# Kernel optimization log

Hardware: AMD Instinct MI355X
Metric: run time of the kernel (lower is better)

Reference implementation:

```python
import jax, jax.numpy as jnp
import numpy as np

# tcnn Hash-grid config from TropicalHashGrid.__init__ defaults
L = 16          # n_levels
F = 2           # n_features_per_level
T = 19          # log2_hashmap_size
N_MIN = 16      # base_resolution
N_MAX = 2048
SCALE = 1.0
HASHMAP = 1 << T
B = 2.0 ** (np.log2(N_MAX * SCALE / N_MIN) / (L - 1))  # per-level scale
PRIMES = np.array([1, 2654435761, 805459861], dtype=np.uint32)
# 8 trilinear corner offsets in {0,1}^3
CORNERS = np.stack(np.meshgrid(*([np.arange(2)] * 3), indexing='ij'), axis=-1).reshape(8, 3)
N_POINTS = 2 ** 21


def _level_encode(x, tbl, scale, res, dense):
    """One hash-grid level: x [N,3], tbl [HASHMAP,F] -> [N,F]."""
    pos = x * scale + 0.5                      # tcnn convention
    pf = jnp.floor(pos)
    frac = pos - pf                            # [N,3]
    grid = pf.astype(jnp.int32)                # [N,3]
    idx = grid[:, None, :] + jnp.asarray(CORNERS, jnp.int32)[None]  # [N,8,3]
    if dense:
        # coarse level fits densely: stride indexing x + y*res + z*res^2
        idx = jnp.minimum(idx, res - 1)
        flat = idx[..., 0] + idx[..., 1] * res + idx[..., 2] * (res * res)
    else:
        # spatial hash: xor of coordinate * prime, masked to table size
        u = idx.astype(jnp.uint32)
        flat = ((u[..., 0] * PRIMES[0]) ^ (u[..., 1] * PRIMES[1]) ^ (u[..., 2] * PRIMES[2]))
        flat = (flat & jnp.uint32(HASHMAP - 1)).astype(jnp.int32)
    feats = tbl[flat]                          # [N,8,F] gather
    c = jnp.asarray(CORNERS, jnp.float32)
    w = jnp.prod(jnp.where(c[None] > 0, frac[:, None, :], 1.0 - frac[:, None, :]), axis=-1)  # [N,8]
    return jnp.einsum('nc,ncf->nf', w, feats)  # trilinear blend


def setup_inputs() -> dict:
    key = jax.random.key(0)
    k1, k2 = jax.random.split(key)
    x = jax.random.uniform(k1, (N_POINTS, 3), dtype=jnp.float32)  # coords in [0,1)^3
    # hash table params (tcnn inits ~U(-1e-4,1e-4); scaled randn equivalent scale)
    table = jax.random.normal(k2, (L, HASHMAP, F), dtype=jnp.float32) * 1e-4
    return {"x": x, "table": table}


def reference(x, table):
    outs = []
    for l in range(L):
        scale = float(N_MIN * (B ** l) - 1.0)   # grid_scale per tcnn/_marks
        res = int(np.ceil(scale)) + 1
        dense = (res ** 3) <= HASHMAP
        outs.append(_level_encode(x, table[l], scale, res, dense))
    return jnp.concatenate(outs, axis=-1)        # [N, L*F]
```

## Files before the change

kernel.cpp:

```cpp
#include <hip/hip_runtime.h>
#include <cstdint>
#include <cmath>


typedef float    f32x2 __attribute__((ext_vector_type(2)));
typedef float    f32x4 __attribute__((ext_vector_type(4)));
typedef uint32_t u32x2 __attribute__((ext_vector_type(2)));
typedef uint32_t u32x4 __attribute__((ext_vector_type(4)));
typedef _Float16 h16x2 __attribute__((ext_vector_type(2)));

#define NLEVELS 16
#define HASHMAP (1 << 19)
#define HMASK ((uint32_t)(HASHMAP - 1))
#define PRIME_Y 2654435761u
#define PRIME_Z 805459861u
#define F16SCALE 1024.0f
#define F16UNSCALE (1.0f / 1024.0f)

struct HGParams {
    float scale[NLEVELS];
    int   res[NLEVELS];
    int   dense[NLEVELS];
    int   dpk_off[NLEVELS];
    int   hq_off[NLEVELS];
    int   dq_off[NLEVELS];
};

__device__ __forceinline__ uint32_t sel4(u32x4 q, uint32_t k) {
    const uint32_t a = (k & 1u) ? q.y : q.x;
    const uint32_t b = (k & 1u) ? q.w : q.z;
    return (k & 2u) ? b : a;
}
__device__ __forceinline__ void unpack_h2(uint32_t w, float& lo, float& hi) {
    const h16x2 h = __builtin_bit_cast(h16x2, w);
    lo = (float)h.x; hi = (float)h.y;
}
__device__ __forceinline__ uint32_t pack_h2(float a, float b) {
    h16x2 h; h.x = (_Float16)a; h.y = (_Float16)b;
    return __builtin_bit_cast(uint32_t, h);
}

__global__ __launch_bounds__(256) void repack_hashed_f16(
    const f32x4* __restrict__ table2, uint32_t* __restrict__ hqw, HGParams p)
{
    const int l = blockIdx.y;
    if (p.hq_off[l] < 0) return;
    const f32x4* __restrict__ src = table2 + (size_t)l * (HASHMAP / 2);
    u32x2* __restrict__ dst = (u32x2*)(hqw + (size_t)p.hq_off[l] * 4);
    for (int k = blockIdx.x * 256 + threadIdx.x; k < HASHMAP / 2;
         k += gridDim.x * 256) {
        const f32x4 v = src[k];
        u32x2 w;
        w.x = pack_h2(v.x * F16SCALE, v.y * F16SCALE);
        w.y = pack_h2(v.z * F16SCALE, v.w * F16SCALE);
        dst[k] = w;
    }
}

__global__ __launch_bounds__(256) void repack_dense_f16(
    const f32x2* __restrict__ table, u32x4* __restrict__ dqt, HGParams p)
{
    const int l = blockIdx.y;
    if (p.dq_off[l] < 0) return;
    const int res = p.res[l];
    const int rm = res - 1;
    const int r2 = res * res;
    const int res3 = r2 * res;
    const f32x2* __restrict__ src = table + (size_t)l * HASHMAP;
    u32x4* __restrict__ dst = dqt + p.dq_off[l];
    for (int k = blockIdx.x * 256 + threadIdx.x; k < res3;
         k += gridDim.x * 256) {
        const int x = k % res;
        const int t = k / res;
        const int y = t % res;
        const int dx = (x < rm) ? 1 : 0;
        const int dy = (y < rm) ? res : 0;
        const f32x2 e00 = src[k];
        const f32x2 e10 = src[k + dx];
        const f32x2 e01 = src[k + dy];
        const f32x2 e11 = src[k + dx + dy];
        u32x4 w;
        w.x = pack_h2(e00.x * F16SCALE, e00.y * F16SCALE);
        w.y = pack_h2(e10.x * F16SCALE, e10.y * F16SCALE);
        w.z = pack_h2(e01.x * F16SCALE, e01.y * F16SCALE);
        w.w = pack_h2(e11.x * F16SCALE, e11.y * F16SCALE);
        dst[k] = w;
    }
}

__global__ __launch_bounds__(256) void repack_dense_k(
    const f32x2* __restrict__ table, f32x4* __restrict__ dpk, HGParams p)
{
    const int l = blockIdx.y;
    if (!p.dense[l] || p.dpk_off[l] < 0) return;
    const int res = p.res[l];
    const int res3 = res * res * res;
    const f32x2* __restrict__ src = table + (size_t)l * HASHMAP;
    f32x4* __restrict__ dst = dpk + p.dpk_off[l];
    for (int k = blockIdx.x * 256 + threadIdx.x; k < res3; k += gridDim.x * 256) {
        const f32x2 a = src[k];
        const f32x2 b = src[k + 1];
        f32x4 v; v.x = a.x; v.y = a.y; v.z = b.x; v.w = b.y;
        dst[k] = v;
    }
}

__global__ __launch_bounds__(256) void hashgrid_level(
    const float* __restrict__ x,
    const float* __restrict__ table,
    const f32x4* __restrict__ dpk,
    const u32x4* __restrict__ hq,
    const u32x4* __restrict__ dq,
    f32x2* __restrict__ dst,
    HGParams p,
    int npoints,
    size_t stride_l,
    size_t stride_n)
{
    __shared__ float sx[768];
    const int tid = threadIdx.x;
    const int base = blockIdx.x << 8;
    const int l = blockIdx.y;

    const int total = npoints * 3;
#pragma unroll
    for (int k = 0; k < 3; ++k) {
        const int li = tid + (k << 8);
        const int gi = base * 3 + li;
        sx[li] = (gi < total) ? x[gi] : 0.0f;
    }
    __syncthreads();

    const int n = base + tid;
    if (n >= npoints) return;

    const float scale = p.scale[l];
    const int   res   = p.res[l];
    const bool  dense = (p.dense[l] != 0);

    const float px = sx[tid * 3 + 0] * scale + 0.5f;
    const float py = sx[tid * 3 + 1] * scale + 0.5f;
    const float pz = sx[tid * 3 + 2] * scale + 0.5f;
    const float fx = floorf(px), fy = floorf(py), fz = floorf(pz);
    const float rx = px - fx,  ry = py - fy,  rz = pz - fz;
    const int ix = (int)fx, iy = (int)fy, iz = (int)fz;

    const f32x2* __restrict__ tbl =
        (const f32x2*)table + (size_t)l * (size_t)HASHMAP;

    const float wx0 = 1.0f - rx, wx1 = rx;
    const float wy_[2] = {1.0f - ry, ry};
    const float wz_[2] = {1.0f - rz, rz};

    float ax = 0.0f, ay = 0.0f;
    float osc = 1.0f;

    if (dense) {
        const int rm = res - 1;
        const int x0 = min(ix, rm);
        const int y0 = min(iy, rm);
        const int z0 = min(iz, rm), z1 = min(iz + 1, rm);
        const int r2 = res * res;
        if (dq && p.dq_off[l] >= 0) {
            osc = F16UNSCALE;
            const u32x4* __restrict__ dt = dq + p.dq_off[l];
            const int b = x0 + y0 * res;
            const u32x4 qa = dt[b + z0 * r2];
            const u32x4 qb = dt[b + z1 * r2];
            const float wy0 = wy_[0], wy1 = wy_[1];
            float a00x, a00y, a10x, a10y, a01x, a01y, a11x, a11y;
            unpack_h2(qa.x, a00x, a00y);
            unpack_h2(qa.y, a10x, a10y);
            unpack_h2(qa.z, a01x, a01y);
            unpack_h2(qa.w, a11x, a11y);
            const float bax = wy0 * (wx0 * a00x + wx1 * a10x)
                            + wy1 * (wx0 * a01x + wx1 * a11x);
            const float bay = wy0 * (wx0 * a00y + wx1 * a10y)
                            + wy1 * (wx0 * a01y + wx1 * a11y);
            float b00x, b00y, b10x, b10y, b01x, b01y, b11x, b11y;
            unpack_h2(qb.x, b00x, b00y);
            unpack_h2(qb.y, b10x, b10y);
            unpack_h2(qb.z, b01x, b01y);
            unpack_h2(qb.w, b11x, b11y);
            const float bbx = wy0 * (wx0 * b00x + wx1 * b10x)
                            + wy1 * (wx0 * b01x + wx1 * b11x);
            const float bby = wy0 * (wx0 * b00y + wx1 * b10y)
                            + wy1 * (wx0 * b01y + wx1 * b11y);
            ax = wz_[0] * bax + wz_[1] * bbx;
            ay = wz_[0] * bay + wz_[1] * bby;
        } else {
            const int x1 = min(ix + 1, rm);
            const int yy1 = min(iy + 1, rm);
            const int ys[2] = {y0 * res, yy1 * res};
            const int zs[2] = {z0 * r2,  z1 * r2};
            const int d = x1 - x0;
            if (dpk && p.dpk_off[l] >= 0) {
                const f32x4* __restrict__ dt = dpk + p.dpk_off[l];
                f32x4 f4[4];
#pragma unroll
                for (int c = 0; c < 4; ++c)
                    f4[c] = dt[x0 + ys[(c >> 1) & 1] + zs[c & 1]];
#pragma unroll
                for (int c = 0; c < 4; ++c) {
                    const f32x2 c0 = f4[c].xy;
                    const f32x2 c1 = d ? f4[c].zw : f4[c].xy;
                    const float wyz = wy_[(c >> 1) & 1] * wz_[c & 1];
                    ax += wyz * (wx0 * c0.x + wx1 * c1.x);
                    ay += wyz * (wx0 * c0.y + wx1 * c1.y);
                }
            } else {
                f32x2 f0[4], f1[4];
#pragma unroll
                for (int c = 0; c < 4; ++c) {
                    const int b = ys[(c >> 1) & 1] + zs[c & 1];
                    f0[c] = tbl[x0 + b];
                    f1[c] = tbl[x1 + b];
                }
#pragma unroll
                for (int c = 0; c < 4; ++c) {
                    const float wyz = wy_[(c >> 1) & 1] * wz_[c & 1];
                    ax += wyz * (wx0 * f0[c].x + wx1 * f1[c].x);
                    ay += wyz * (wx0 * f0[c].y + wx1 * f1[c].y);
                }
            }
        }
    } else {
        const uint32_t ux = (uint32_t)ix;
        const uint32_t hy[2] = {(uint32_t)iy * PRIME_Y, (uint32_t)(iy + 1) * PRIME_Y};
        const uint32_t hz[2] = {(uint32_t)iz * PRIME_Z, (uint32_t)(iz + 1) * PRIME_Z};

        uint32_t H0[4], H1[4];
#pragma unroll
        for (int c = 0; c < 4; ++c) {
            const uint32_t hyz = hy[(c >> 1) & 1] ^ hz[c & 1];
            H0[c] = (ux ^ hyz) & HMASK;
            H1[c] = ((ux + 1u) ^ hyz) & HMASK;
        }

        if (hq && p.hq_off[l] >= 0) {
            osc = F16UNSCALE;
            const u32x4* __restrict__ ht = hq + p.hq_off[l];
            u32x4 q0[4];
#pragma unroll
            for (int c = 0; c < 4; ++c) q0[c] = ht[H0[c] >> 2];
            const bool straddle = ((ux & 3u) == 3u);
            u32x4 q1[4];
            if (straddle) {
#pragma unroll
                for (int c = 0; c < 4; ++c) q1[c] = ht[H1[c] >> 2];
            }
#pragma unroll
            for (int c = 0; c < 4; ++c) {
                const uint32_t e0 = sel4(q0[c], H0[c] & 3u);
                uint32_t e1;
                if (straddle) e1 = sel4(q1[c], H1[c] & 3u);
                else          e1 = sel4(q0[c], H1[c] & 3u);
                float c0x, c0y, c1x, c1y;
                unpack_h2(e0, c0x, c0y);
                unpack_h2(e1, c1x, c1y);
                const float wyz = wy_[(c >> 1) & 1] * wz_[c & 1];
                ax += wyz * (wx0 * c0x + wx1 * c1x);
                ay += wyz * (wx0 * c0y + wx1 * c1y);
            }
        } else {
            const f32x4* __restrict__ t4 = (const f32x4*)tbl;
            f32x4 f4[4];
#pragma unroll
            for (int c = 0; c < 4; ++c) f4[c] = t4[H0[c] >> 1];
            f32x2 c1v[4];
            if (ux & 1u) {
#pragma unroll
                for (int c = 0; c < 4; ++c) c1v[c] = tbl[H1[c]];
            } else {
#pragma unroll
                for (int c = 0; c < 4; ++c)
                    c1v[c] = (H0[c] & 1u) ? f4[c].xy : f4[c].zw;
            }
#pragma unroll
            for (int c = 0; c < 4; ++c) {
                const f32x2 c0 = (H0[c] & 1u) ? f4[c].zw : f4[c].xy;
                const float wyz = wy_[(c >> 1) & 1] * wz_[c & 1];
                ax += wyz * (wx0 * c0.x + wx1 * c1v[c].x);
                ay += wyz * (wx0 * c0.y + wx1 * c1v[c].y);
            }
        }
    }

    f32x2 acc; acc.x = ax * osc; acc.y = ay * osc;
    __builtin_nontemporal_store(acc, dst + (size_t)l * stride_l + (size_t)n * stride_n);
}

__global__ __launch_bounds__(256) void transpose_out(
    const f32x4* __restrict__ ws4,
    f32x4* __restrict__ out4,
    int npoints)
{
    __shared__ f32x2 tile[NLEVELS][130];
    const int tid = threadIdx.x;
    const int base = blockIdx.x << 7;
    const int np2 = npoints >> 1;

#pragma unroll
    for (int k = 0; k < 4; ++k) {
        const int flat = tid + (k << 8);
        const int l  = flat >> 6;
        const int pr = flat & 63;
        const int gp = (base >> 1) + pr;
        if (gp < np2) {
            const f32x4 v = __builtin_nontemporal_load(ws4 + (size_t)l * np2 + gp);
            tile[l][2 * pr]     = v.xy;
            tile[l][2 * pr + 1] = v.zw;
        }
    }
    __syncthreads();

#pragma unroll
    for (int k = 0; k < 4; ++k) {
        const int flat = tid + (k << 8);
        const int nl = flat >> 3;
        const int c  = flat & 7;
        const int nn = base + nl;
        if (nn < npoints) {
            const f32x2 a = tile[2 * c][nl];
            const f32x2 b = tile[2 * c + 1][nl];
            f32x4 v; v.x = a.x; v.y = a.y; v.z = b.x; v.w = b.y;
            __builtin_nontemporal_store(v, out4 + (size_t)nn * 8 + c);
        }
    }
}

extern "C" void kernel_launch(void* const* d_in, const int* in_sizes, int n_in,
                              void* d_out, int out_size, void* d_ws, size_t ws_size,
                              hipStream_t stream) {
    const float* x     = (const float*)d_in[0];
    const float* table = (const float*)d_in[1];
    float* out         = (float*)d_out;
    const int npoints  = in_sizes[0] / 3;

    HGParams p;
    const double B = pow(2.0, 7.0 / 15.0);
    int dpk_total = 0;
    int dq_total = 0;
    int hq_total = 0;
    int max_res3 = 0;
    for (int l = 0; l < NLEVELS; ++l) {
        const double s = 16.0 * pow(B, (double)l) - 1.0;
        p.scale[l] = (float)s;
        const int res = (int)ceil(s) + 1;
        p.res[l] = res;
        const long long r3 = (long long)res * res * res;
        p.dense[l] = (r3 <= (long long)HASHMAP) ? 1 : 0;
        if (p.dense[l]) {
            p.dpk_off[l] = dpk_total;  dpk_total += (int)r3;
            p.dq_off[l]  = dq_total;   dq_total  += (int)r3;
            p.hq_off[l]  = -1;
            if ((int)r3 > max_res3) max_res3 = (int)r3;
        } else {
            p.dpk_off[l] = -1;
            p.dq_off[l]  = -1;
            p.hq_off[l]  = hq_total;   hq_total  += HASHMAP / 4;
        }
    }

    const size_t need_main = (size_t)npoints * NLEVELS * sizeof(f32x2);
    const bool ws_main = (ws_size >= need_main) && ((npoints & 1) == 0);
    const size_t off0 = ws_main ? need_main : 0;

    const size_t hq_bytes = (size_t)hq_total * 16;
    const size_t dq_bytes = (size_t)dq_total * 16;
    const bool tierA = (ws_size >= off0 + hq_bytes + dq_bytes);

    const u32x4* hq = nullptr;
    const u32x4* dq = nullptr;
    const f32x4* dpk = nullptr;

    if (tierA) {
        uint32_t* hqw = (uint32_t*)((char*)d_ws + off0);
        u32x4*    dqt = (u32x4*)((char*)d_ws + off0 + hq_bytes);
        hq = (const u32x4*)hqw;
        dq = dqt;
        {
            const dim3 gr(1024, NLEVELS);
            repack_hashed_f16<<<gr, 256, 0, stream>>>(
                (const f32x4*)table, hqw, p);
        }
        {
            const dim3 gr((max_res3 + 255) / 256, NLEVELS);
            repack_dense_f16<<<gr, 256, 0, stream>>>(
                (const f32x2*)table, dqt, p);
        }
    } else {
        for (int l = 0; l < NLEVELS; ++l) { p.hq_off[l] = -1; p.dq_off[l] = -1; }
        const size_t need_dpk = (size_t)dpk_total * sizeof(f32x4);
        const bool use_dpk = (ws_size >= off0 + need_dpk) && dpk_total > 0;
        if (use_dpk) {
            f32x4* dpkw = (f32x4*)((char*)d_ws + off0);
            dpk = dpkw;
            const dim3 gr((max_res3 + 255) / 256, NLEVELS);
            repack_dense_k<<<gr, 256, 0, stream>>>((const f32x2*)table, dpkw, p);
        } else {
            for (int l = 0; l < NLEVELS; ++l) p.dpk_off[l] = -1;
        }
    }

    const dim3 g1((npoints + 255) / 256, NLEVELS);
    if (ws_main) {
        hashgrid_level<<<g1, 256, 0, stream>>>(
            x, table, dpk, hq, dq, (f32x2*)d_ws, p, npoints,
            (size_t)npoints, (size_t)1);
        const int nb2 = (npoints + 127) / 128;
        transpose_out<<<nb2, 256, 0, stream>>>(
            (const f32x4*)d_ws, (f32x4*)out, npoints);
    } else {
        hashgrid_level<<<g1, 256, 0, stream>>>(
            x, table, dpk, hq, dq, (f32x2*)out, p, npoints,
            (size_t)1, (size_t)NLEVELS);
    }
}
```

Measured before the change: 929.3 us.

## Process two points per thread to raise memory-level parallelism in hash gathers

Each thread now handles two consecutive points, issuing all gathers for both before blending so more loads are in flight per thread. The fp16 hashed path fetches only the single extra word on a straddle (via XOR of the x-delta) instead of a second full 16-byte row. Output is written as one 16-byte store when contiguous, and launch bounds request 8 waves per EU. This raises register pressure and halves the thread count, which may reduce latency hiding.

Result: slower. 1.020 ms (+9.7%).

```diff
diff --git a/kernel.cpp b/kernel.cpp
--- a/kernel.cpp
+++ b/kernel.cpp
@@ -105,7 +105,89 @@
     }
 }
 
-__global__ __launch_bounds__(256) void hashgrid_level(
+__device__ __forceinline__ void point_fp32(
+    const f32x2* __restrict__ tbl, const f32x4* __restrict__ dpkt,
+    bool dense, int res,
+    float rx, float ry, float rz, int ix, int iy, int iz,
+    float& ox, float& oy)
+{
+    const float wx0 = 1.0f - rx, wx1 = rx;
+    const float wy_[2] = {1.0f - ry, ry};
+    const float wz_[2] = {1.0f - rz, rz};
+    float ax = 0.0f, ay = 0.0f;
+    if (dense) {
+        const int rm = res - 1;
+        const int x0 = min(ix, rm), x1 = min(ix + 1, rm);
+        const int y0 = min(iy, rm), y1 = min(iy + 1, rm);
+        const int z0 = min(iz, rm), z1 = min(iz + 1, rm);
+        const int r2 = res * res;
+        const int ys[2] = {y0 * res, y1 * res};
+        const int zs[2] = {z0 * r2,  z1 * r2};
+        const int d = x1 - x0;
+        if (dpkt) {
+            f32x4 f4[4];
+#pragma unroll
+            for (int c = 0; c < 4; ++c)
+                f4[c] = dpkt[x0 + ys[(c >> 1) & 1] + zs[c & 1]];
+#pragma unroll
+            for (int c = 0; c < 4; ++c) {
+                const f32x2 c0 = f4[c].xy;
+                const f32x2 c1 = d ? f4[c].zw : f4[c].xy;
+                const float wyz = wy_[(c >> 1) & 1] * wz_[c & 1];
+                ax += wyz * (wx0 * c0.x + wx1 * c1.x);
+                ay += wyz * (wx0 * c0.y + wx1 * c1.y);
+            }
+        } else {
+            f32x2 f0[4], f1[4];
+#pragma unroll
+            for (int c = 0; c < 4; ++c) {
+                const int b = ys[(c >> 1) & 1] + zs[c & 1];
+                f0[c] = tbl[x0 + b];
+                f1[c] = tbl[x1 + b];
+            }
+#pragma unroll
+            for (int c = 0; c < 4; ++c) {
+                const float wyz = wy_[(c >> 1) & 1] * wz_[c & 1];
+                ax += wyz * (wx0 * f0[c].x + wx1 * f1[c].x);
+                ay += wyz * (wx0 * f0[c].y + wx1 * f1[c].y);
+            }
+        }
+    } else {
+        const uint32_t ux = (uint32_t)ix;
+        const uint32_t hy[2] = {(uint32_t)iy * PRIME_Y, (uint32_t)(iy + 1) * PRIME_Y};
+        const uint32_t hz[2] = {(uint32_t)iz * PRIME_Z, (uint32_t)(iz + 1) * PRIME_Z};
+        uint32_t H0[4], H1[4];
+#pragma unroll
+        for (int c = 0; c < 4; ++c) {
+            const uint32_t hyz = hy[(c >> 1) & 1] ^ hz[c & 1];
+            H0[c] = (ux ^ hyz) & HMASK;
+            H1[c] = ((ux + 1u) ^ hyz) & HMASK;
+        }
+        const f32x4* __restrict__ t4 = (const f32x4*)tbl;
+        f32x4 f4[4];
+#pragma unroll
+        for (int c = 0; c < 4; ++c) f4[c] = t4[H0[c] >> 1];
+        f32x2 c1v[4];
+        if (ux & 1u) {
+#pragma unroll
+            for (int c = 0; c < 4; ++c) c1v[c] = tbl[H1[c]];
+        } else {
+#pragma unroll
+            for (int c = 0; c < 4; ++c)
+                c1v[c] = (H0[c] & 1u) ? f4[c].xy : f4[c].zw;
+        }
+#pragma unroll
+        for (int c = 0; c < 4; ++c) {
+            const f32x2 c0 = (H0[c] & 1u) ? f4[c].zw : f4[c].xy;
+            const float wyz = wy_[(c >> 1) & 1] * wz_[c & 1];
+            ax += wyz * (wx0 * c0.x + wx1 * c1v[c].x);
+            ay += wyz * (wx0 * c0.y + wx1 * c1v[c].y);
+        }
+    }
+    ox = ax; oy = ay;
+}
+
+__global__ __launch_bounds__(256, 8) void hashgrid_level(
     const float* __restrict__ x,
     const float* __restrict__ table,
     const f32x4* __restrict__ dpk,
@@ -117,177 +199,163 @@
     size_t stride_l,
     size_t stride_n)
 {
-    __shared__ float sx[768];
+    __shared__ float sx[1536];
     const int tid = threadIdx.x;
-    const int base = blockIdx.x << 8;
+    const int base = blockIdx.x << 9;
     const int l = blockIdx.y;
 
     const int total = npoints * 3;
-#pragma unroll
-    for (int k = 0; k < 3; ++k) {
+    const int sbase = base * 3;
+#pragma unroll
+    for (int k = 0; k < 6; ++k) {
         const int li = tid + (k << 8);
-        const int gi = base * 3 + li;
+        const int gi = sbase + li;
         sx[li] = (gi < total) ? x[gi] : 0.0f;
     }
     __syncthreads();
 
-    const int n = base + tid;
-    if (n >= npoints) return;
+    const int n0 = base + (tid << 1);
+    if (n0 >= npoints) return;
+    const bool pair = (n0 + 1) < npoints;
 
     const float scale = p.scale[l];
     const int   res   = p.res[l];
     const bool  dense = (p.dense[l] != 0);
 
-    const float px = sx[tid * 3 + 0] * scale + 0.5f;
-    const float py = sx[tid * 3 + 1] * scale + 0.5f;
-    const float pz = sx[tid * 3 + 2] * scale + 0.5f;
-    const float fx = floorf(px), fy = floorf(py), fz = floorf(pz);
-    const float rx = px - fx,  ry = py - fy,  rz = pz - fz;
-    const int ix = (int)fx, iy = (int)fy, iz = (int)fz;
-
-    const f32x2* __restrict__ tbl =
-        (const f32x2*)table + (size_t)l * (size_t)HASHMAP;
-
-    const float wx0 = 1.0f - rx, wx1 = rx;
-    const float wy_[2] = {1.0f - ry, ry};
-    const float wz_[2] = {1.0f - rz, rz};
-
-    float ax = 0.0f, ay = 0.0f;
-    float osc = 1.0f;
-
-    if (dense) {
-        const int rm = res - 1;
-        const int x0 = min(ix, rm);
-        const int y0 = min(iy, rm);
-        const int z0 = min(iz, rm), z1 = min(iz + 1, rm);
-        const int r2 = res * res;
-        if (dq && p.dq_off[l] >= 0) {
-            osc = F16UNSCALE;
-            const u32x4* __restrict__ dt = dq + p.dq_off[l];
+    float rx[2], ry[2], rz[2];
+    int ixv[2], iyv[2], izv[2];
+#pragma unroll
+    for (int j = 0; j < 2; ++j) {
+        const int s = ((tid << 1) | j) * 3;
+        const float px = sx[s + 0] * scale + 0.5f;
+        const float py = sx[s + 1] * scale + 0.5f;
+        const float pz = sx[s + 2] * scale + 0.5f;
+        const float fx = floorf(px), fy = floorf(py), fz = floorf(pz);
+        rx[j] = px - fx; ry[j] = py - fy; rz[j] = pz - fz;
+        ixv[j] = (int)fx; iyv[j] = (int)fy; izv[j] = (int)fz;
+    }
+
+    float ox[2], oy[2];
+
+    if (dense && dq && p.dq_off[l] >= 0) {
+        const u32x4* __restrict__ dt = dq + p.dq_off[l];
+        const int rm = res - 1, r2 = res * res;
+        u32x4 qa[2], qb[2];
+#pragma unroll
+        for (int j = 0; j < 2; ++j) {
+            const int x0 = min(ixv[j], rm), y0 = min(iyv[j], rm);
+            const int z0 = min(izv[j], rm), z1 = min(izv[j] + 1, rm);
             const int b = x0 + y0 * res;
-            const u32x4 qa = dt[b + z0 * r2];
-            const u32x4 qb = dt[b + z1 * r2];
-            const float wy0 = wy_[0], wy1 = wy_[1];
+            qa[j] = dt[b + z0 * r2];
+            qb[j] = dt[b + z1 * r2];
+        }
+#pragma unroll
+        for (int j = 0; j < 2; ++j) {
+            const float wx0 = 1.0f - rx[j], wx1 = rx[j];
+            const float wy0 = 1.0f - ry[j], wy1 = ry[j];
+            const float wz0 = 1.0f - rz[j], wz1 = rz[j];
             float a00x, a00y, a10x, a10y, a01x, a01y, a11x, a11y;
-            unpack_h2(qa.x, a00x, a00y);
-            unpack_h2(qa.y, a10x, a10y);
-            unpack_h2(qa.z, a01x, a01y);
-            unpack_h2(qa.w, a11x, a11y);
+            unpack_h2(qa[j].x, a00x, a00y);
+            unpack_h2(qa[j].y, a10x, a10y);
+            unpack_h2(qa[j].z, a01x, a01y);
+            unpack_h2(qa[j].w, a11x, a11y);
             const float bax = wy0 * (wx0 * a00x + wx1 * a10x)
                             + wy1 * (wx0 * a01x + wx1 * a11x);
             const float bay = wy0 * (wx0 * a00y + wx1 * a10y)
                             + wy1 * (wx0 * a01y + wx1 * a11y);
             float b00x, b00y, b10x, b10y, b01x, b01y, b11x, b11y;
-            unpack_h2(qb.x, b00x, b00y);
-            unpack_h2(qb.y, b10x, b10y);
-            unpack_h2(qb.z, b01x, b01y);
-            unpack_h2(qb.w, b11x, b11y);
+            unpack_h2(qb[j].x, b00x, b00y);
+            unpack_h2(qb[j].y, b10x, b10y);
+            unpack_h2(qb[j].z, b01x, b01y);
+            unpack_h2(qb[j].w, b11x, b11y);
             const float bbx = wy0 * (wx0 * b00x + wx1 * b10x)
                             + wy1 * (wx0 * b01x + wx1 * b11x);
             const float bby = wy0 * (wx0 * b00y + wx1 * b10y)
                             + wy1 * (wx0 * b01y + wx1 * b11y);
-            ax = wz_[0] * bax + wz_[1] * bbx;
-            ay = wz_[0] * bay + wz_[1] * bby;
-        } else {
-            const int x1 = min(ix + 1, rm);
-            const int yy1 = min(iy + 1, rm);
-            const int ys[2] = {y0 * res, yy1 * res};
-            const int zs[2] = {z0 * r2,  z1 * r2};
-            const int d = x1 - x0;
-            if (dpk && p.dpk_off[l] >= 0) {
-                const f32x4* __restrict__ dt = dpk + p.dpk_off[l];
-                f32x4 f4[4];
+            ox[j] = (wz0 * bax + wz1 * bbx) * F16UNSCALE;
+            oy[j] = (wz0 * bay + wz1 * bby) * F16UNSCALE;
+        }
+    } else if (!dense && hq && p.hq_off[l] >= 0) {
+        const u32x4* __restrict__ ht = hq + p.hq_off[l];
+        const uint32_t* __restrict__ htw = (const uint32_t*)ht;
+        uint32_t H0[2][4], dxm[2];
+        bool st[2];
+#pragma unroll
+        for (int j = 0; j < 2; ++j) {
+            const uint32_t ux = (uint32_t)ixv[j];
+            const uint32_t hy0 = (uint32_t)iyv[j] * PRIME_Y;
+            const uint32_t hy1 = (uint32_t)(iyv[j] + 1) * PRIME_Y;
+            const uint32_t hz0 = (uint32_t)izv[j] * PRIME_Z;
+            const uint32_t hz1 = (uint32_t)(izv[j] + 1) * PRIME_Z;
+#pragma unroll
+            for (int c = 0; c < 4; ++c) {
+                const uint32_t hyz = ((c & 2) ? hy1 : hy0) ^ ((c & 1) ? hz1 : hz0);
+                H0[j][c] = (ux ^ hyz) & HMASK;
+            }
+            dxm[j] = (ux ^ (ux + 1u)) & HMASK;
+            st[j] = (dxm[j] >= 4u);
+        }
+        u32x4 q0[2][4];
+#pragma unroll
+        for (int j = 0; j < 2; ++j)
+#pragma unroll
+            for (int c = 0; c < 4; ++c)
+                q0[j][c] = ht[H0[j][c] >> 2];
+        uint32_t sE[2][4];
+#pragma unroll
+        for (int j = 0; j < 2; ++j) {
+            if (st[j]) {
 #pragma unroll
                 for (int c = 0; c < 4; ++c)
-                    f4[c] = dt[x0 + ys[(c >> 1) & 1] + zs[c & 1]];
-#pragma unroll
-                for (int c = 0; c < 4; ++c) {
-                    const f32x2 c0 = f4[c].xy;
-                    const f32x2 c1 = d ? f4[c].zw : f4[c].xy;
-                    const float wyz = wy_[(c >> 1) & 1] * wz_[c & 1];
-                    ax += wyz * (wx0 * c0.x + wx1 * c1.x);
-                    ay += wyz * (wx0 * c0.y + wx1 * c1.y);
-                }
-            } else {
-                f32x2 f0[4], f1[4];
-#pragma unroll
-                for (int c = 0; c < 4; ++c) {
-                    const int b = ys[(c >> 1) & 1] + zs[c & 1];
-                    f0[c] = tbl[x0 + b];
-                    f1[c] = tbl[x1 + b];
-                }
-#pragma unroll
-                for (int c = 0; c < 4; ++c) {
-                    const float wyz = wy_[(c >> 1) & 1] * wz_[c & 1];
-                    ax += wyz * (wx0 * f0[c].x + wx1 * f1[c].x);
-                    ay += wyz * (wx0 * f0[c].y + wx1 * f1[c].y);
-                }
-            }
-        }
-    } else {
-        const uint32_t ux = (uint32_t)ix;
-        const uint32_t hy[2] = {(uint32_t)iy * PRIME_Y, (uint32_t)(iy + 1) * PRIME_Y};
-        const uint32_t hz[2] = {(uint32_t)iz * PRIME_Z, (uint32_t)(iz + 1) * PRIME_Z};
-
-        uint32_t H0[4], H1[4];
-#pragma unroll
-        for (int c = 0; c < 4; ++c) {
-            const uint32_t hyz = hy[(c >> 1) & 1] ^ hz[c & 1];
-            H0[c] = (ux ^ hyz) & HMASK;
-            H1[c] = ((ux + 1u) ^ hyz) & HMASK;
-        }
-
-        if (hq && p.hq_off[l] >= 0) {
-            osc = F16UNSCALE;
-            const u32x4* __restrict__ ht = hq + p.hq_off[l];
-            u32x4 q0[4];
-#pragma unroll
-            for (int c = 0; c < 4; ++c) q0[c] = ht[H0[c] >> 2];
-            const bool straddle = ((ux & 3u) == 3u);
-            u32x4 q1[4];
-            if (straddle) {
-#pragma unroll
-                for (int c = 0; c < 4; ++c) q1[c] = ht[H1[c] >> 2];
-            }
+                    sE[j][c] = htw[H0[j][c] ^ dxm[j]];
+            }
+        }
+#pragma unroll
+        for (int j = 0; j < 2; ++j) {
+            const float wx0 = 1.0f - rx[j], wx1 = rx[j];
+            const float wy0 = 1.0f - ry[j], wy1 = ry[j];
+            const float wz0 = 1.0f - rz[j], wz1 = rz[j];
+            float ax = 0.0f, ay = 0.0f;
 #pragma unroll
             for (int c = 0; c < 4; ++c) {
-                const uint32_t e0 = sel4(q0[c], H0[c] & 3u);
-                uint32_t e1;
-                if (straddle) e1 = sel4(q1[c], H1[c] & 3u);
-                else          e1 = sel4(q0[c], H1[c] & 3u);
+                const uint32_t k0 = H0[j][c] & 3u;
+                const uint32_t e0 = sel4(q0[j][c], k0);
+                const uint32_t e1 = st[j] ? sE[j][c]
+                                          : sel4(q0[j][c], k0 ^ (dxm[j] & 3u));
                 float c0x, c0y, c1x, c1y;
                 unpack_h2(e0, c0x, c0y);
                 unpack_h2(e1, c1x, c1y);
-                const float wyz = wy_[(c >> 1) & 1] * wz_[c & 1];
+                const float wyz = ((c & 2) ? wy1 : wy0) * ((c & 1) ? wz1 : wz0);
                 ax += wyz * (wx0 * c0x + wx1 * c1x);
                 ay += wyz * (wx0 * c0y + wx1 * c1y);
             }
-        } else {
-            const f32x4* __restrict__ t4 = (const f32x4*)tbl;
-            f32x4 f4[4];
-#pragma unroll
-            for (int c = 0; c < 4; ++c) f4[c] = t4[H0[c] >> 1];
-            f32x2 c1v[4];
-            if (ux & 1u) {
-#pragma unroll
-                for (int c = 0; c < 4; ++c) c1v[c] = tbl[H1[c]];
-            } else {
-#pragma unroll
-                for (int c = 0; c < 4; ++c)
-                    c1v[c] = (H0[c] & 1u) ? f4[c].xy : f4[c].zw;
-            }
-#pragma unroll
-            for (int c = 0; c < 4; ++c) {
-                const f32x2 c0 = (H0[c] & 1u) ? f4[c].zw : f4[c].xy;
-                const float wyz = wy_[(c >> 1) & 1] * wz_[c & 1];
-                ax += wyz * (wx0 * c0.x + wx1 * c1v[c].x);
-                ay += wyz * (wx0 * c0.y + wx1 * c1v[c].y);
-            }
-        }
-    }
-
-    f32x2 acc; acc.x = ax * osc; acc.y = ay * osc;
-    __builtin_nontemporal_store(acc, dst + (size_t)l * stride_l + (size_t)n * stride_n);
+            ox[j] = ax * F16UNSCALE;
+            oy[j] = ay * F16UNSCALE;
+        }
+    } else {
+        const f32x2* __restrict__ tbl =
+            (const f32x2*)table + (size_t)l * (size_t)HASHMAP;
+        const f32x4* __restrict__ dpkt =
+            (dense && dpk && p.dpk_off[l] >= 0) ? (dpk + p.dpk_off[l]) : nullptr;
+#pragma unroll
+        for (int j = 0; j < 2; ++j)
+            point_fp32(tbl, dpkt, dense, res,
+                       rx[j], ry[j], rz[j], ixv[j], iyv[j], izv[j],
+                       ox[j], oy[j]);
+    }
+
+    const size_t db = (size_t)l * stride_l;
+    if (pair && stride_n == 1) {
+        f32x4 v; v.x = ox[0]; v.y = oy[0]; v.z = ox[1]; v.w = oy[1];
+        __builtin_nontemporal_store(v, (f32x4*)(dst + db + (size_t)n0));
+    } else {
+        f32x2 a; a.x = ox[0]; a.y = oy[0];
+        __builtin_nontemporal_store(a, dst + db + (size_t)n0 * stride_n);
+        if (pair) {
+            f32x2 b2; b2.x = ox[1]; b2.y = oy[1];
+            __builtin_nontemporal_store(b2, dst + db + (size_t)(n0 + 1) * stride_n);
+        }
+    }
 }
 
 __global__ __launch_bounds__(256) void transpose_out(
@@ -403,7 +471,7 @@
         }
     }
 
-    const dim3 g1((npoints + 255) / 256, NLEVELS);
+    const dim3 g1((npoints + 511) / 512, NLEVELS);
     if (ws_main) {
         hashgrid_level<<<g1, 256, 0, stream>>>(
             x, table, dpk, hq, dq, (f32x2*)d_ws, p, npoints,
```
